# Kernel tuning notes

Measured on AMD Instinct MI355X. Metric: run time of the kernel, lower is better.

The kernel has to match this reference:

```python
import jax, jax.numpy as jnp
import numpy as np

DIM = 1024
H = 16          # query heads
HKV = 4         # kv heads
HD = DIM // H   # head_dim = 64
B = 8           # equal-length docs
S = 1024        # tokens per doc
N = B * S       # total tokens
ROPE_BASE = 10000.0


def _rms_norm(x, scale):
    eps = jnp.asarray(jnp.finfo(x.dtype).eps, x.dtype)
    inv = jax.lax.rsqrt(jnp.mean(x * x, axis=-1, keepdims=True) + eps)
    return x * inv * scale


def _rope(x, cos, sin):
    # x: [N, h, HD]; cos/sin: [N, 1, HD//2]
    half = x.shape[-1] // 2
    x1, x2 = x[..., :half], x[..., half:]
    return jnp.concatenate((x1 * cos + x2 * sin, -x1 * sin + x2 * cos), axis=-1)


def setup_inputs() -> dict:
    key = jax.random.key(0)
    ks = jax.random.split(key, 8)
    x = jax.random.normal(ks[0], (N, DIM), dtype=jnp.float32)
    Wq = jax.random.normal(ks[1], (DIM, DIM), dtype=jnp.float32) * (DIM ** -0.5)
    Wk = jax.random.normal(ks[2], (HKV * HD, DIM), dtype=jnp.float32) * (DIM ** -0.5)
    Wv = jax.random.normal(ks[3], (HKV * HD, DIM), dtype=jnp.float32) * (DIM ** -0.5)
    Wproj = jax.random.normal(ks[4], (DIM, DIM), dtype=jnp.float32) * (DIM ** -0.5)
    q_gain = jnp.full((H,), 1.0, dtype=jnp.float32)
    q_scale = jnp.asarray(1.0, dtype=jnp.float32)  # q RMSNorm scale
    k_scale = jnp.asarray(1.0, dtype=jnp.float32)  # k RMSNorm scale
    # rotary tables per Rotary.prepare_positions (positions reset per doc)
    cu_seqlens = jnp.arange(B + 1, dtype=jnp.int32) * S
    positions = jnp.tile(jnp.arange(S, dtype=jnp.float32), B)  # [N]
    inv_freq = 1.0 / (ROPE_BASE ** (jnp.arange(0, HD, 2, dtype=jnp.float32) / HD))
    freqs = positions[:, None] * inv_freq[None, :]  # [N, HD//2]
    rotary_cos = jnp.cos(freqs)[:, None, :]
    rotary_sin = jnp.sin(freqs)[:, None, :]
    return {
        "x": x, "Wq": Wq, "Wk": Wk, "Wv": Wv, "Wproj": Wproj,
        "q_gain": q_gain, "q_scale": q_scale, "k_scale": k_scale,
        "rotary_cos": rotary_cos, "rotary_sin": rotary_sin,
        "cu_seqlens": cu_seqlens, "max_doc_len": S,
    }


def reference(x, Wq, Wk, Wv, Wproj, q_gain, q_scale, k_scale,
              rotary_cos, rotary_sin, cu_seqlens, max_doc_len):
    n_tokens, dim = x.shape
    q = (x @ Wq.T).reshape(n_tokens, H, HD)
    k = (x @ Wk.T).reshape(n_tokens, HKV, HD)
    v = (x @ Wv.T).reshape(n_tokens, HKV, HD)
    q = _rms_norm(q, q_scale)
    k = _rms_norm(k, k_scale)
    q = _rope(q, rotary_cos, rotary_sin)
    k = _rope(k, rotary_cos, rotary_sin)
    q = q * q_gain[None, :, None]
    # equal-length docs -> [B, S, h, HD]; GQA: repeat kv heads
    rep = H // HKV
    qb = q.reshape(B, S, H, HD)
    kb = jnp.repeat(k.reshape(B, S, HKV, HD), rep, axis=2)
    vb = jnp.repeat(v.reshape(B, S, HKV, HD), rep, axis=2)
    scale = HD ** -0.5
    scores = jnp.einsum('bqhd,bkhd->bhqk', qb, kb) * scale  # [B,H,S,S]
    causal = jnp.tril(jnp.ones((S, S), dtype=bool))
    scores = jnp.where(causal[None, None], scores, jnp.asarray(-jnp.inf, scores.dtype))
    attn = jax.nn.softmax(scores, axis=-1)
    y = jnp.einsum('bhqk,bkhd->bqhd', attn, vb).reshape(n_tokens, dim)
    return y @ Wproj.T
```

## Files before the change

kernel.cpp:

```cpp
#include <hip/hip_runtime.h>
#include <hip/hip_bf16.h>


typedef __bf16 bf16x8 __attribute__((ext_vector_type(8)));
typedef float f32x4 __attribute__((ext_vector_type(4)));

__device__ __forceinline__ void async16(const void* g, void* l) {
  __builtin_amdgcn_global_load_lds((const __attribute__((address_space(1))) void*)g,
                                   (__attribute__((address_space(3))) void*)l, 16, 0, 0);
}

__device__ __forceinline__ unsigned short f2bfu(float x) {
  __hip_bfloat16 h = __float2bfloat16(x);
  return __builtin_bit_cast(unsigned short, h);
}

__global__ __launch_bounds__(256) void castall(
    const float4* __restrict__ x, const float4* __restrict__ Wq,
    const float4* __restrict__ Wk, const float4* __restrict__ Wv,
    const float4* __restrict__ Wp,
    ushort4* __restrict__ xb, ushort4* __restrict__ w1b, ushort4* __restrict__ wpb) {
  int i = blockIdx.x * 256 + threadIdx.x;
  const float4* src;
  ushort4* dst;
  if (i < 2097152)      { src = x + i;             dst = xb + i; }
  else if (i < 2359296) { src = Wq + (i - 2097152); dst = w1b + (i - 2097152); }
  else if (i < 2424832) { src = Wk + (i - 2359296); dst = w1b + (i - 2097152); }
  else if (i < 2490368) { src = Wv + (i - 2424832); dst = w1b + (i - 2097152); }
  else                  { src = Wp + (i - 2490368); dst = wpb + (i - 2490368); }
  float4 v = *src;
  ushort4 o;
  o.x = f2bfu(v.x); o.y = f2bfu(v.y); o.z = f2bfu(v.z); o.w = f2bfu(v.w);
  *dst = o;
}

__global__ __launch_bounds__(256, 3) void gemm_qkv(
    const __hip_bfloat16* __restrict__ A,
    const __hip_bfloat16* __restrict__ Bm,
    const float* __restrict__ cosb, const float* __restrict__ sinb,
    const float* __restrict__ qgain, const float* __restrict__ qscale,
    const float* __restrict__ kscale,
    __hip_bfloat16* __restrict__ Qo,
    __hip_bfloat16* __restrict__ Ko,
    __hip_bfloat16* __restrict__ Vo)
{
  __shared__ __align__(16) unsigned short As[128 * 32];
  __shared__ __align__(16) unsigned short Bs[128 * 32];
  const int tid = threadIdx.x;
  const int wave = tid >> 6, lane = tid & 63;
  const int quad = lane >> 4, l15 = lane & 15;
  const int bn = blockIdx.x, bm = blockIdx.y;
  const int wm = (wave >> 1) * 64, wn = (wave & 1) * 64;
  const int srow = lane >> 2, scol = (lane & 3) * 8;
  const int K = 1024;

  f32x4 acc[4][4] = {};

  const __hip_bfloat16* Ab = A + (size_t)bm * 128 * K;
  const __hip_bfloat16* Bb = Bm + (size_t)bn * 128 * K;

  for (int kt = 0; kt < K; kt += 32) {
    __syncthreads();
#pragma unroll
    for (int c = 0; c < 2; c++) {
      const int ch = wave * 2 + c;
      async16(Ab + (size_t)(ch * 16 + srow) * K + kt + scol, &As[ch * 512]);
      async16(Bb + (size_t)(ch * 16 + srow) * K + kt + scol, &Bs[ch * 512]);
    }
    __syncthreads();
    bf16x8 af[4], bfr[4];
#pragma unroll
    for (int mt = 0; mt < 4; mt++)
      af[mt] = *(const bf16x8*)&As[(wm + mt * 16 + l15) * 32 + quad * 8];
#pragma unroll
    for (int nt = 0; nt < 4; nt++)
      bfr[nt] = *(const bf16x8*)&Bs[(wn + nt * 16 + l15) * 32 + quad * 8];
#pragma unroll
    for (int mt = 0; mt < 4; mt++)
#pragma unroll
      for (int nt = 0; nt < 4; nt++)
        acc[mt][nt] = __builtin_amdgcn_mfma_f32_16x16x32_bf16(af[mt], bfr[nt], acc[mt][nt], 0, 0, 0);
  }

  const int hg = bn * 2 + (wn >> 6);
  const int tokbase = bm * 128 + wm;

  if (hg >= 20) {
    const int hv = hg - 20;
#pragma unroll
    for (int mt = 0; mt < 4; mt++)
#pragma unroll
      for (int r = 0; r < 4; r++) {
        const int tok = tokbase + mt * 16 + quad * 4 + r;
#pragma unroll
        for (int nt = 0; nt < 4; nt++)
          Vo[(size_t)tok * 256 + hv * 64 + nt * 16 + l15] = __float2bfloat16(acc[mt][nt][r]);
      }
  } else {
    const bool isq = hg < 16;
    const float scale = isq ? qscale[0] : kscale[0];
    const float gain = isq ? qgain[hg] * 0.18033688011112042f : 1.0f;
    const float sg = scale * gain;
#pragma unroll
    for (int mt = 0; mt < 4; mt++) {
      float inv[4];
#pragma unroll
      for (int r = 0; r < 4; r++) {
        float ss = acc[mt][0][r] * acc[mt][0][r] + acc[mt][1][r] * acc[mt][1][r] +
                   acc[mt][2][r] * acc[mt][2][r] + acc[mt][3][r] * acc[mt][3][r];
#pragma unroll
        for (int off = 1; off < 16; off <<= 1) ss += __shfl_xor(ss, off);
        inv[r] = rsqrtf(ss * (1.0f / 64.0f) + 1.1920929e-07f) * sg;
      }
#pragma unroll
      for (int r = 0; r < 4; r++) {
        const int tok = tokbase + mt * 16 + quad * 4 + r;
        const float c0 = cosb[tok * 32 + l15], c1 = cosb[tok * 32 + 16 + l15];
        const float s0 = sinb[tok * 32 + l15], s1 = sinb[tok * 32 + 16 + l15];
        const float v0 = acc[mt][0][r] * inv[r];
        const float v1 = acc[mt][1][r] * inv[r];
        const float v2 = acc[mt][2][r] * inv[r];
        const float v3 = acc[mt][3][r] * inv[r];
        const float o0 = v0 * c0 + v2 * s0;
        const float o1 = v1 * c1 + v3 * s1;
        const float o2 = -v0 * s0 + v2 * c0;
        const float o3 = -v1 * s1 + v3 * c1;
        __hip_bfloat16* base = isq ? (Qo + (size_t)tok * 1024 + hg * 64)
                                   : (Ko + (size_t)tok * 256 + (hg - 16) * 64);
        base[l15]      = __float2bfloat16(o0);
        base[16 + l15] = __float2bfloat16(o1);
        base[32 + l15] = __float2bfloat16(o2);
        base[48 + l15] = __float2bfloat16(o3);
      }
    }
  }
}

__global__ __launch_bounds__(256, 3) void gemm_p(
    const __hip_bfloat16* __restrict__ A,
    const __hip_bfloat16* __restrict__ Bm,
    float* __restrict__ C)
{
  __shared__ __align__(16) unsigned short As[128 * 32];
  __shared__ __align__(16) unsigned short Bs[128 * 32];
  const int tid = threadIdx.x;
  const int wave = tid >> 6, lane = tid & 63;
  const int quad = lane >> 4, l15 = lane & 15;
  const int bn = blockIdx.x, bm = blockIdx.y;
  const int wm = (wave >> 1) * 64, wn = (wave & 1) * 64;
  const int srow = lane >> 2, scol = (lane & 3) * 8;
  const int K = 1024;

  f32x4 acc[4][4] = {};

  const __hip_bfloat16* Ab = A + (size_t)bm * 128 * K;
  const __hip_bfloat16* Bb = Bm + (size_t)bn * 128 * K;

  for (int kt = 0; kt < K; kt += 32) {
    __syncthreads();
#pragma unroll
    for (int c = 0; c < 2; c++) {
      const int ch = wave * 2 + c;
      async16(Ab + (size_t)(ch * 16 + srow) * K + kt + scol, &As[ch * 512]);
      async16(Bb + (size_t)(ch * 16 + srow) * K + kt + scol, &Bs[ch * 512]);
    }
    __syncthreads();
    bf16x8 af[4], bfr[4];
#pragma unroll
    for (int mt = 0; mt < 4; mt++)
      af[mt] = *(const bf16x8*)&As[(wm + mt * 16 + l15) * 32 + quad * 8];
#pragma unroll
    for (int nt = 0; nt < 4; nt++)
      bfr[nt] = *(const bf16x8*)&Bs[(wn + nt * 16 + l15) * 32 + quad * 8];
#pragma unroll
    for (int mt = 0; mt < 4; mt++)
#pragma unroll
      for (int nt = 0; nt < 4; nt++)
        acc[mt][nt] = __builtin_amdgcn_mfma_f32_16x16x32_bf16(af[mt], bfr[nt], acc[mt][nt], 0, 0, 0);
  }

#pragma unroll
  for (int mt = 0; mt < 4; mt++)
#pragma unroll
    for (int r = 0; r < 4; r++) {
      const int row = bm * 128 + wm + mt * 16 + quad * 4 + r;
#pragma unroll
      for (int nt = 0; nt < 4; nt++)
        C[(size_t)row * 1024 + bn * 128 + wn + nt * 16 + l15] = acc[mt][nt][r];
    }
}

__global__ __launch_bounds__(256) void vtrans(const unsigned short* __restrict__ vkb,
                                              unsigned short* __restrict__ Vt) {
  __shared__ unsigned short t[64][65];
  const int st = blockIdx.x, kvh = blockIdx.y, b = blockIdx.z;
  const int tid = threadIdx.x;
  const int s0 = st * 64;
#pragma unroll
  for (int i = 0; i < 16; i++) {
    const int idx = tid + i * 256;
    const int sl = idx >> 6, d = idx & 63;
    t[sl][d] = vkb[(size_t)(b * 1024 + s0 + sl) * 256 + kvh * 64 + d];
  }
  __syncthreads();
#pragma unroll
  for (int i = 0; i < 16; i++) {
    const int idx = tid + i * 256;
    const int d = idx >> 6, sl = idx & 63;
    Vt[((size_t)(b * 4 + kvh) * 64 + d) * 1024 + s0 + sl] = t[sl][d];
  }
}

__global__ __launch_bounds__(256, 2) void attn(
    const __hip_bfloat16* __restrict__ Q,
    const __hip_bfloat16* __restrict__ Kk,
    const __hip_bfloat16* __restrict__ Vt,
    __hip_bfloat16* __restrict__ Y)
{
  __shared__ __align__(16) unsigned short Kb[2][4096];
  __shared__ __align__(16) unsigned short Vb[2][4096];
  __shared__ __align__(16) unsigned short Pm[4][32 * 72];

  const int p = blockIdx.x;
  const int qt_a = 15 - p, qt_b = p;
  const int kvh2 = blockIdx.y;
  const int kvh = kvh2 >> 1, hh = kvh2 & 1;
  const int b = blockIdx.z;
  const int tid = threadIdx.x;
  const int wave = tid >> 6, lane = tid & 63;
  const int quad = lane >> 4, l15 = lane & 15;
  const int h = kvh * 4 + hh * 2 + (wave >> 1);
  const int m0 = (wave & 1) * 32;
  const int srow = lane >> 2, scol = (lane & 3) * 8;

  auto issue = [&](int kt, unsigned short* Ks, unsigned short* Vs) {
#pragma unroll
    for (int c = 0; c < 4; c++) {
      const int ch = wave * 4 + c;
      const int v = ch >> 3;
      const int ch8 = ch & 7;
      const int kc = ch8 >> 2, grp = ch8 & 3;
      if (v == 0)
        async16(Kk + (size_t)(b * 1024 + kt * 64 + grp * 16 + srow) * 256 + kvh * 64 + kc * 32 + scol,
                Ks + kc * 2048 + grp * 512 + lane * 8);
      else
        async16(Vt + ((size_t)((b * 4 + kvh) * 64 + grp * 16 + srow)) * 1024 + kt * 64 + kc * 32 + scol,
                Vs + kc * 2048 + grp * 512 + lane * 8);
    }
  };

  bf16x8 qf[2][2];
  {
    const int tok0 = b * 1024 + qt_a * 64;
#pragma unroll
    for (int mt = 0; mt < 2; mt++)
#pragma unroll
      for (int kc = 0; kc < 2; kc++)
        qf[mt][kc] = *(const bf16x8*)(Q + (size_t)(tok0 + m0 + mt * 16 + l15) * 1024 +
                                      h * 64 + kc * 32 + quad * 8);
  }

  issue(0, Kb[0], Vb[0]);

  f32x4 of[2][4] = {};
  f32x4 lf[2] = {};
  unsigned short* Pw = Pm[wave];

  bf16x8 onesf;
#pragma unroll
  for (int j = 0; j < 8; j++) onesf[j] = (__bf16)1.0f;

  const int steps_a = qt_a + 1;
  const int total = steps_a + qt_b + 1;

  for (int g = 0; g < total; ++g) {
    const bool pa = g < steps_a;
    const int qtc = pa ? qt_a : qt_b;
    const int kt = pa ? g : g - steps_a;

    __syncthreads();
    if (g + 1 < total) {
      const int gn = g + 1;
      const int ktn = (gn < steps_a) ? gn : gn - steps_a;
      issue(ktn, Kb[gn & 1], Vb[gn & 1]);
    }
    if (g == steps_a) {
      const int tok0 = b * 1024 + qt_b * 64;
#pragma unroll
      for (int mt = 0; mt < 2; mt++)
#pragma unroll
        for (int kc = 0; kc < 2; kc++)
          qf[mt][kc] = *(const bf16x8*)(Q + (size_t)(tok0 + m0 + mt * 16 + l15) * 1024 +
                                        h * 64 + kc * 32 + quad * 8);
    }
    const unsigned short* Ks = Kb[g & 1];
    const unsigned short* Vs = Vb[g & 1];

    f32x4 sf[4][2] = {};
    __builtin_amdgcn_s_setprio(1);
#pragma unroll
    for (int kc = 0; kc < 2; kc++) {
#pragma unroll
      for (int kk = 0; kk < 4; kk++) {
        const bf16x8 kf = *(const bf16x8*)&Ks[kc * 2048 + (kk * 16 + l15) * 32 + quad * 8];
#pragma unroll
        for (int mt = 0; mt < 2; mt++)
          sf[kk][mt] = __builtin_amdgcn_mfma_f32_16x16x32_bf16(kf, qf[mt][kc], sf[kk][mt], 0, 0, 0);
      }
    }
    __builtin_amdgcn_s_setprio(0);

    const bool diag = (kt == qtc);
#pragma unroll
    for (int mt = 0; mt < 2; mt++) {
#pragma unroll
      for (int kk = 0; kk < 4; kk++) {
        ushort4 pk;
        unsigned short* pp = (unsigned short*)&pk;
#pragma unroll
        for (int r = 0; r < 4; r++) {
          float pv;
          if (diag && (kk * 16 + quad * 4 + r) > (m0 + mt * 16 + l15))
            pv = 0.0f;
          else
            pv = __builtin_amdgcn_exp2f(sf[kk][mt][r]);
          pp[r] = f2bfu(pv);
        }
        *(ushort4*)&Pw[(mt * 16 + l15) * 72 + kk * 16 + quad * 4] = pk;
      }
    }

    asm volatile("s_waitcnt lgkmcnt(0)" ::: "memory");

    __builtin_amdgcn_s_setprio(1);
#pragma unroll
    for (int kc = 0; kc < 2; kc++) {
#pragma unroll
      for (int mt = 0; mt < 2; mt++) {
        const bf16x8 ap = *(const bf16x8*)&Pw[(mt * 16 + l15) * 72 + kc * 32 + quad * 8];
        lf[mt] = __builtin_amdgcn_mfma_f32_16x16x32_bf16(ap, onesf, lf[mt], 0, 0, 0);
#pragma unroll
        for (int dt = 0; dt < 4; dt++) {
          const bf16x8 bv = *(const bf16x8*)&Vs[kc * 2048 + (dt * 16 + l15) * 32 + quad * 8];
          of[mt][dt] = __builtin_amdgcn_mfma_f32_16x16x32_bf16(ap, bv, of[mt][dt], 0, 0, 0);
        }
      }
    }
    __builtin_amdgcn_s_setprio(0);

    if (diag) {
      const int tok0 = b * 1024 + qtc * 64;
#pragma unroll
      for (int mt = 0; mt < 2; mt++)
#pragma unroll
        for (int r = 0; r < 4; r++) {
          const float rcp = 1.0f / lf[mt][r];
          const int row = tok0 + m0 + mt * 16 + quad * 4 + r;
#pragma unroll
          for (int dt = 0; dt < 4; dt++)
            Y[(size_t)row * 1024 + h * 64 + dt * 16 + l15] = __float2bfloat16(of[mt][dt][r] * rcp);
        }
      if (pa) {
#pragma unroll
        for (int mt = 0; mt < 2; mt++) {
          lf[mt] = f32x4{0.f, 0.f, 0.f, 0.f};
#pragma unroll
          for (int dt = 0; dt < 4; dt++) of[mt][dt] = f32x4{0.f, 0.f, 0.f, 0.f};
        }
      }
    }
  }
}

extern "C" void kernel_launch(void* const* d_in, const int* in_sizes, int n_in,
                              void* d_out, int out_size, void* d_ws, size_t ws_size,
                              hipStream_t stream) {
  const float* x      = (const float*)d_in[0];
  const float* Wq     = (const float*)d_in[1];
  const float* Wk     = (const float*)d_in[2];
  const float* Wv     = (const float*)d_in[3];
  const float* Wp     = (const float*)d_in[4];
  const float* qgain  = (const float*)d_in[5];
  const float* qscale = (const float*)d_in[6];
  const float* kscale = (const float*)d_in[7];
  const float* cosb   = (const float*)d_in[8];
  const float* sinb   = (const float*)d_in[9];
  float* out = (float*)d_out;
  char* ws = (char*)d_ws;

  __hip_bfloat16* xb  = (__hip_bfloat16*)(ws);
  __hip_bfloat16* w1b = (__hip_bfloat16*)(ws + 16777216);
  __hip_bfloat16* wpb = (__hip_bfloat16*)(ws + 19922944);
  __hip_bfloat16* qb  = (__hip_bfloat16*)(ws + 22020096);
  __hip_bfloat16* kb  = (__hip_bfloat16*)(ws + 38797312);
  __hip_bfloat16* vkb = (__hip_bfloat16*)(ws + 42991616);
  __hip_bfloat16* vtb = (__hip_bfloat16*)(ws + 47185920);
  __hip_bfloat16* yb  = (__hip_bfloat16*)(ws + 51380224);

  castall<<<10752, 256, 0, stream>>>((const float4*)x, (const float4*)Wq, (const float4*)Wk,
                                     (const float4*)Wv, (const float4*)Wp,
                                     (ushort4*)xb, (ushort4*)w1b, (ushort4*)wpb);

  gemm_qkv<<<dim3(12, 64), 256, 0, stream>>>(xb, w1b, cosb, sinb, qgain, qscale, kscale,
                                             qb, kb, vkb);

  vtrans<<<dim3(16, 4, 8), 256, 0, stream>>>((const unsigned short*)vkb, (unsigned short*)vtb);

  attn<<<dim3(8, 8, 8), 256, 0, stream>>>(qb, kb, vtb, yb);

  gemm_p<<<dim3(8, 64), 256, 0, stream>>>(yb, wpb, out);
}
```

Before: 211.0 us.

## Double GEMM K-tile to 64 with XOR-swizzled LDS and XCD-aware block remap

Both bf16 GEMMs (QKV projection and output projection) now stage a K-tile of 64 instead of 32 per iteration. This halves the number of barrier pairs per K loop. LDS rows are XOR-swizzled by row index so the 128-byte-wide rows avoid bank conflicts on the bf16x8 fragment reads. The launch grid is flattened and remapped so consecutive blocks on each of the 8 XCDs share A/B tiles for better L2 reuse. LDS per block doubles to 32KB, which may limit occupancy, and there is still no double buffering.

```diff
diff --git a/kernel.cpp b/kernel.cpp
--- a/kernel.cpp
+++ b/kernel.cpp
@@ -44,14 +44,17 @@
     __hip_bfloat16* __restrict__ Ko,
     __hip_bfloat16* __restrict__ Vo)
 {
-  __shared__ __align__(16) unsigned short As[128 * 32];
-  __shared__ __align__(16) unsigned short Bs[128 * 32];
+  __shared__ __align__(16) unsigned short As[128 * 64];
+  __shared__ __align__(16) unsigned short Bs[128 * 64];
   const int tid = threadIdx.x;
   const int wave = tid >> 6, lane = tid & 63;
   const int quad = lane >> 4, l15 = lane & 15;
-  const int bn = blockIdx.x, bm = blockIdx.y;
+  const int flat = blockIdx.x;
+  const int swz = (flat & 7) * 96 + (flat >> 3);
+  const int bn = swz % 12, bm = swz / 12;
   const int wm = (wave >> 1) * 64, wn = (wave & 1) * 64;
-  const int srow = lane >> 2, scol = (lane & 3) * 8;
+  const int srow = lane >> 3;
+  const int scol = ((lane & 7) ^ srow) * 8;
   const int K = 1024;
 
   f32x4 acc[4][4] = {};
@@ -59,27 +62,34 @@
   const __hip_bfloat16* Ab = A + (size_t)bm * 128 * K;
   const __hip_bfloat16* Bb = Bm + (size_t)bn * 128 * K;
 
-  for (int kt = 0; kt < K; kt += 32) {
+  for (int kt = 0; kt < K; kt += 64) {
     __syncthreads();
 #pragma unroll
-    for (int c = 0; c < 2; c++) {
-      const int ch = wave * 2 + c;
-      async16(Ab + (size_t)(ch * 16 + srow) * K + kt + scol, &As[ch * 512]);
-      async16(Bb + (size_t)(ch * 16 + srow) * K + kt + scol, &Bs[ch * 512]);
+    for (int c = 0; c < 4; c++) {
+      const int ch = wave * 4 + c;
+      async16(Ab + (size_t)(ch * 8 + srow) * K + kt + scol, &As[ch * 512]);
+      async16(Bb + (size_t)(ch * 8 + srow) * K + kt + scol, &Bs[ch * 512]);
     }
     __syncthreads();
-    bf16x8 af[4], bfr[4];
-#pragma unroll
-    for (int mt = 0; mt < 4; mt++)
-      af[mt] = *(const bf16x8*)&As[(wm + mt * 16 + l15) * 32 + quad * 8];
-#pragma unroll
-    for (int nt = 0; nt < 4; nt++)
-      bfr[nt] = *(const bf16x8*)&Bs[(wn + nt * 16 + l15) * 32 + quad * 8];
-#pragma unroll
-    for (int mt = 0; mt < 4; mt++)
-#pragma unroll
-      for (int nt = 0; nt < 4; nt++)
-        acc[mt][nt] = __builtin_amdgcn_mfma_f32_16x16x32_bf16(af[mt], bfr[nt], acc[mt][nt], 0, 0, 0);
+#pragma unroll
+    for (int ks = 0; ks < 2; ks++) {
+      bf16x8 af[4], bfr[4];
+#pragma unroll
+      for (int mt = 0; mt < 4; mt++) {
+        const int row = wm + mt * 16 + l15;
+        af[mt] = *(const bf16x8*)&As[row * 64 + (((ks << 2) + quad) ^ (row & 7)) * 8];
+      }
+#pragma unroll
+      for (int nt = 0; nt < 4; nt++) {
+        const int row = wn + nt * 16 + l15;
+        bfr[nt] = *(const bf16x8*)&Bs[row * 64 + (((ks << 2) + quad) ^ (row & 7)) * 8];
+      }
+#pragma unroll
+      for (int mt = 0; mt < 4; mt++)
+#pragma unroll
+        for (int nt = 0; nt < 4; nt++)
+          acc[mt][nt] = __builtin_amdgcn_mfma_f32_16x16x32_bf16(af[mt], bfr[nt], acc[mt][nt], 0, 0, 0);
+    }
   }
 
   const int hg = bn * 2 + (wn >> 6);
@@ -141,14 +151,17 @@
     const __hip_bfloat16* __restrict__ Bm,
     float* __restrict__ C)
 {
-  __shared__ __align__(16) unsigned short As[128 * 32];
-  __shared__ __align__(16) unsigned short Bs[128 * 32];
+  __shared__ __align__(16) unsigned short As[128 * 64];
+  __shared__ __align__(16) unsigned short Bs[128 * 64];
   const int tid = threadIdx.x;
   const int wave = tid >> 6, lane = tid & 63;
   const int quad = lane >> 4, l15 = lane & 15;
-  const int bn = blockIdx.x, bm = blockIdx.y;
+  const int flat = blockIdx.x;
+  const int swz = (flat & 7) * 64 + (flat >> 3);
+  const int bn = swz & 7, bm = swz >> 3;
   const int wm = (wave >> 1) * 64, wn = (wave & 1) * 64;
-  const int srow = lane >> 2, scol = (lane & 3) * 8;
+  const int srow = lane >> 3;
+  const int scol = ((lane & 7) ^ srow) * 8;
   const int K = 1024;
 
   f32x4 acc[4][4] = {};
@@ -156,27 +169,34 @@
   const __hip_bfloat16* Ab = A + (size_t)bm * 128 * K;
   const __hip_bfloat16* Bb = Bm + (size_t)bn * 128 * K;
 
-  for (int kt = 0; kt < K; kt += 32) {
+  for (int kt = 0; kt < K; kt += 64) {
     __syncthreads();
 #pragma unroll
-    for (int c = 0; c < 2; c++) {
-      const int ch = wave * 2 + c;
-      async16(Ab + (size_t)(ch * 16 + srow) * K + kt + scol, &As[ch * 512]);
-      async16(Bb + (size_t)(ch * 16 + srow) * K + kt + scol, &Bs[ch * 512]);
+    for (int c = 0; c < 4; c++) {
+      const int ch = wave * 4 + c;
+      async16(Ab + (size_t)(ch * 8 + srow) * K + kt + scol, &As[ch * 512]);
+      async16(Bb + (size_t)(ch * 8 + srow) * K + kt + scol, &Bs[ch * 512]);
     }
     __syncthreads();
-    bf16x8 af[4], bfr[4];
-#pragma unroll
-    for (int mt = 0; mt < 4; mt++)
-      af[mt] = *(const bf16x8*)&As[(wm + mt * 16 + l15) * 32 + quad * 8];
-#pragma unroll
-    for (int nt = 0; nt < 4; nt++)
-      bfr[nt] = *(const bf16x8*)&Bs[(wn + nt * 16 + l15) * 32 + quad * 8];
-#pragma unroll
-    for (int mt = 0; mt < 4; mt++)
-#pragma unroll
-      for (int nt = 0; nt < 4; nt++)
-        acc[mt][nt] = __builtin_amdgcn_mfma_f32_16x16x32_bf16(af[mt], bfr[nt], acc[mt][nt], 0, 0, 0);
+#pragma unroll
+    for (int ks = 0; ks < 2; ks++) {
+      bf16x8 af[4], bfr[4];
+#pragma unroll
+      for (int mt = 0; mt < 4; mt++) {
+        const int row = wm + mt * 16 + l15;
+        af[mt] = *(const bf16x8*)&As[row * 64 + (((ks << 2) + quad) ^ (row & 7)) * 8];
+      }
+#pragma unroll
+      for (int nt = 0; nt < 4; nt++) {
+        const int row = wn + nt * 16 + l15;
+        bfr[nt] = *(const bf16x8*)&Bs[row * 64 + (((ks << 2) + quad) ^ (row & 7)) * 8];
+      }
+#pragma unroll
+      for (int mt = 0; mt < 4; mt++)
+#pragma unroll
+        for (int nt = 0; nt < 4; nt++)
+          acc[mt][nt] = __builtin_amdgcn_mfma_f32_16x16x32_bf16(af[mt], bfr[nt], acc[mt][nt], 0, 0, 0);
+    }
   }
 
 #pragma unroll
@@ -401,12 +421,12 @@
                                      (const float4*)Wv, (const float4*)Wp,
                                      (ushort4*)xb, (ushort4*)w1b, (ushort4*)wpb);
 
-  gemm_qkv<<<dim3(12, 64), 256, 0, stream>>>(xb, w1b, cosb, sinb, qgain, qscale, kscale,
-                                             qb, kb, vkb);
+  gemm_qkv<<<768, 256, 0, stream>>>(xb, w1b, cosb, sinb, qgain, qscale, kscale,
+                                    qb, kb, vkb);
 
   vtrans<<<dim3(16, 4, 8), 256, 0, stream>>>((const unsigned short*)vkb, (unsigned short*)vtb);
 
   attn<<<dim3(8, 8, 8), 256, 0, stream>>>(qb, kb, vtb, yb);
 
-  gemm_p<<<dim3(8, 64), 256, 0, stream>>>(yb, wpb, out);
-}
+  gemm_p<<<512, 256, 0, stream>>>(yb, wpb, out);
+}
```

Measured after the change: 196.5 us. 6.9% less time.
